# Kernel optimization log

Hardware: AMD Instinct MI355X
Metric: run time of the kernel (lower is better)

Reference implementation:

```python
import jax, jax.numpy as jnp
import numpy as np

N_OBJECTS = 32  # mask labels 1..32 (0 = background)


def setup_inputs() -> dict:
    key = jax.random.key(0)
    k1, k2, k3, k4 = jax.random.split(key, 4)
    B, F, H, W = 8, 64, 256, 256
    encoded = jax.random.normal(k1, (B, F, H, W), dtype=jnp.float32)
    masks = jax.random.randint(k2, (B, 1, H, W), 0, N_OBJECTS + 1, dtype=jnp.int32)
    W1 = jax.random.normal(k3, (2 * F, F // 2), dtype=jnp.float32) * 0.05
    b1 = jnp.zeros((F // 2,), dtype=jnp.float32)
    W2 = jax.random.normal(k4, (F // 2, 4), dtype=jnp.float32) * 0.05
    b2 = jnp.zeros((4,), dtype=jnp.float32)
    return {"encoded": encoded, "masks": masks, "W1": W1, "b1": b1, "W2": W2, "b2": b2}


def reference(encoded, masks, W1, b1, W2, b2):
    B, F, H, W = encoded.shape
    # --- masked per-object max-pool (segment max over pixels) ---
    enc = encoded.reshape(B, F, H * W).transpose(0, 2, 1)  # [B, HW, F]
    ids = masks.reshape(B, H * W)                          # [B, HW]
    seg_max = jax.vmap(
        lambda d, i: jax.ops.segment_max(d, i, num_segments=N_OBJECTS + 1)
    )(enc, ids)                                            # [B, N+1, F]
    vectors = seg_max[:, 1:, :]                            # [B, N, F] (skip label 0)

    # --- O(N^2) pairwise MLP: connections[b,c,j,i] = sigmoid(MLP([v_i; v_j])) ---
    N = vectors.shape[1]
    vi = jnp.broadcast_to(vectors[:, :, None, :], (B, N, N, F))  # v_i over axis 1
    vj = jnp.broadcast_to(vectors[:, None, :, :], (B, N, N, F))  # v_j over axis 2
    pairs = jnp.concatenate([vi, vj], axis=-1)                   # [B, N, N, 2F]
    h = jnp.einsum('bijd,dh->bijh', pairs, W1) + b1
    out = jax.nn.sigmoid(jnp.einsum('bijh,hc->bijc', h, W2) + b2)  # [B, Ni, Nj, C]
    connections = out.transpose(0, 3, 2, 1)                        # [B, C, Nj, Ni]
    return vectors, connections
```

## Files before the change

kernel.cpp:

```cpp
#include <hip/hip_runtime.h>
#include <math.h>

#define B_    8
#define F_    64
#define HW_   65536
#define NSEG  33
#define NOBJ  32
#define CHUNK 1024
#define CPB   (HW_ / CHUNK)
#define ENC_NEG_INF 0x007FFFFFu

__device__ __forceinline__ unsigned enc_f(float x) {
    unsigned u = __float_as_uint(x);
    return u ^ ((unsigned)((int)u >> 31) | 0x80000000u);
}
__device__ __forceinline__ float dec_f(unsigned e) {
    unsigned x = (e & 0x80000000u) ? (e ^ 0x80000000u) : ~e;
    return __uint_as_float(x);
}

__global__ void init_ws(unsigned* __restrict__ gws) {
    int i = blockIdx.x * blockDim.x + threadIdx.x;
    if (i < B_ * NSEG * F_) gws[i] = ENC_NEG_INF;
}

__global__ __launch_bounds__(256) void segmax_kernel(
        const float* __restrict__ enc, const int* __restrict__ masks,
        unsigned* __restrict__ gws) {
    __shared__ unsigned acc[F_ * NSEG];
    const int tid   = threadIdx.x;
    const int b     = blockIdx.x / CPB;
    const int chunk = blockIdx.x % CPB;

    for (int i = tid; i < F_ * NSEG; i += 256) acc[i] = ENC_NEG_INF;

    const int4 ids = ((const int4*)(masks + b * HW_ + chunk * CHUNK))[tid];
    __syncthreads();

    const float4* p = (const float4*)(enc + (size_t)b * F_ * HW_ + chunk * CHUNK) + tid;
    #pragma unroll 4
    for (int f = 0; f < F_; ++f) {
        float4 v = p[(size_t)f * (HW_ / 4)];
        unsigned* a = acc + f * NSEG;
        atomicMax(a + ids.x, enc_f(v.x));
        atomicMax(a + ids.y, enc_f(v.y));
        atomicMax(a + ids.z, enc_f(v.z));
        atomicMax(a + ids.w, enc_f(v.w));
    }
    __syncthreads();

    unsigned* gb = gws + b * (NSEG * F_);
    for (int i = tid; i < F_ * NSEG; i += 256) {
        unsigned val = acc[i];
        if (val != ENC_NEG_INF) {
            int f = i / NSEG, s = i % NSEG;
            atomicMax(gb + s * F_ + f, val);
        }
    }
}

__global__ __launch_bounds__(256) void mlp_kernel(
        const unsigned* __restrict__ gws,
        const float* __restrict__ W1, const float* __restrict__ b1,
        const float* __restrict__ W2, const float* __restrict__ b2,
        float* __restrict__ out_vec, float* __restrict__ out_conn) {
    const int b = blockIdx.x;
    const int tid = threadIdx.x;
    __shared__ float v[NOBJ * F_];
    __shared__ float Am[NOBJ * 33];
    __shared__ float Bm[NOBJ * 33];

    for (int i = tid; i < NOBJ * F_; i += 256) {
        int s = (i >> 6) + 1, f = i & 63;
        float val = dec_f(gws[b * NSEG * F_ + s * F_ + f]);
        v[i] = val;
        out_vec[b * NOBJ * F_ + i] = val;
    }
    __syncthreads();

    for (int e = tid; e < 2 * NOBJ * 32; e += 256) {
        int half = e >> 10;
        int idx  = e & 1023;
        int i = idx >> 5, k = idx & 31;
        const float* vv = v + i * F_;
        const float* w  = W1 + (half ? F_ * 32 : 0) + k;
        float s = 0.f;
        #pragma unroll
        for (int f = 0; f < F_; ++f) s = fmaf(vv[f], w[f * 32], s);
        if (half) Bm[i * 33 + k] = s;
        else      Am[i * 33 + k] = s + b1[k];
    }
    __syncthreads();

    for (int e = tid; e < NOBJ * NOBJ; e += 256) {
        int i = e >> 5, j = e & 31;
        float o0 = b2[0], o1 = b2[1], o2 = b2[2], o3 = b2[3];
        #pragma unroll
        for (int k = 0; k < 32; ++k) {
            float h = Am[i * 33 + k] + Bm[j * 33 + k];
            o0 = fmaf(h, W2[k * 4 + 0], o0);
            o1 = fmaf(h, W2[k * 4 + 1], o1);
            o2 = fmaf(h, W2[k * 4 + 2], o2);
            o3 = fmaf(h, W2[k * 4 + 3], o3);
        }
        float* oc = out_conn + (size_t)b * 4 * NOBJ * NOBJ + j * NOBJ + i;
        oc[0 * NOBJ * NOBJ] = 1.f / (1.f + expf(-o0));
        oc[1 * NOBJ * NOBJ] = 1.f / (1.f + expf(-o1));
        oc[2 * NOBJ * NOBJ] = 1.f / (1.f + expf(-o2));
        oc[3 * NOBJ * NOBJ] = 1.f / (1.f + expf(-o3));
    }
}

extern "C" void kernel_launch(void* const* d_in, const int* in_sizes, int n_in,
                              void* d_out, int out_size, void* d_ws, size_t ws_size,
                              hipStream_t stream) {
    const float* enc   = (const float*)d_in[0];
    const int*   masks = (const int*)  d_in[1];
    const float* W1    = (const float*)d_in[2];
    const float* b1    = (const float*)d_in[3];
    const float* W2    = (const float*)d_in[4];
    const float* b2    = (const float*)d_in[5];

    float* out_vec  = (float*)d_out;
    float* out_conn = out_vec + B_ * NOBJ * F_;
    unsigned* gws   = (unsigned*)d_ws;

    const int n = B_ * NSEG * F_;
    init_ws<<<(n + 255) / 256, 256, 0, stream>>>(gws);
    segmax_kernel<<<B_ * CPB, 256, 0, stream>>>(enc, masks, gws);
    mlp_kernel<<<B_, 256, 0, stream>>>(gws, W1, b1, W2, b2, out_vec, out_conn);
}
```

Before: 250.6 us.

## Split segmax over feature groups, batch loads, and skip redundant atomics

```diff
diff --git a/kernel.cpp b/kernel.cpp
--- a/kernel.cpp
+++ b/kernel.cpp
@@ -8,6 +8,8 @@
 #define NOBJ  32
 #define CHUNK 1024
 #define CPB   (HW_ / CHUNK)
+#define FPB   16
+#define FGRP  (F_ / FPB)
 #define ENC_NEG_INF 0x007FFFFFu
 
 __device__ __forceinline__ unsigned enc_f(float x) {
@@ -24,37 +26,49 @@
     if (i < B_ * NSEG * F_) gws[i] = ENC_NEG_INF;
 }
 
-__global__ __launch_bounds__(256) void segmax_kernel(
+__global__ __launch_bounds__(256, 6) void segmax_kernel(
         const float* __restrict__ enc, const int* __restrict__ masks,
         unsigned* __restrict__ gws) {
-    __shared__ unsigned acc[F_ * NSEG];
-    const int tid   = threadIdx.x;
-    const int b     = blockIdx.x / CPB;
-    const int chunk = blockIdx.x % CPB;
+    __shared__ unsigned acc[FPB * NSEG];
+    const int tid = threadIdx.x;
+    const int blk = blockIdx.x;
+    const int b     = blk >> 8;
+    const int r     = blk & 255;
+    const int chunk = r >> 2;
+    const int fg    = r & 3;
 
-    for (int i = tid; i < F_ * NSEG; i += 256) acc[i] = ENC_NEG_INF;
+    for (int i = tid; i < FPB * NSEG; i += 256) acc[i] = ENC_NEG_INF;
 
     const int4 ids = ((const int4*)(masks + b * HW_ + chunk * CHUNK))[tid];
     __syncthreads();
 
-    const float4* p = (const float4*)(enc + (size_t)b * F_ * HW_ + chunk * CHUNK) + tid;
-    #pragma unroll 4
-    for (int f = 0; f < F_; ++f) {
-        float4 v = p[(size_t)f * (HW_ / 4)];
-        unsigned* a = acc + f * NSEG;
-        atomicMax(a + ids.x, enc_f(v.x));
-        atomicMax(a + ids.y, enc_f(v.y));
-        atomicMax(a + ids.z, enc_f(v.z));
-        atomicMax(a + ids.w, enc_f(v.w));
+    const float4* p = (const float4*)(enc + (size_t)b * F_ * HW_
+                                      + (size_t)(fg * FPB) * HW_
+                                      + chunk * CHUNK) + tid;
+    for (int fo = 0; fo < FPB; fo += 8) {
+        float4 vbuf[8];
+        #pragma unroll
+        for (int u = 0; u < 8; ++u)
+            vbuf[u] = p[(size_t)(fo + u) * (HW_ / 4)];
+        #pragma unroll
+        for (int u = 0; u < 8; ++u) {
+            unsigned* a = acc + (fo + u) * NSEG;
+            unsigned e;
+            e = enc_f(vbuf[u].x); if (e > a[ids.x]) atomicMax(a + ids.x, e);
+            e = enc_f(vbuf[u].y); if (e > a[ids.y]) atomicMax(a + ids.y, e);
+            e = enc_f(vbuf[u].z); if (e > a[ids.z]) atomicMax(a + ids.z, e);
+            e = enc_f(vbuf[u].w); if (e > a[ids.w]) atomicMax(a + ids.w, e);
+        }
     }
     __syncthreads();
 
     unsigned* gb = gws + b * (NSEG * F_);
-    for (int i = tid; i < F_ * NSEG; i += 256) {
+    for (int i = tid; i < FPB * NSEG; i += 256) {
         unsigned val = acc[i];
         if (val != ENC_NEG_INF) {
-            int f = i / NSEG, s = i % NSEG;
-            atomicMax(gb + s * F_ + f, val);
+            int f = i / NSEG + fg * FPB, s = i % NSEG;
+            unsigned* cell = gb + s * F_ + f;
+            if (val > *cell) atomicMax(cell, val);
         }
     }
 }
@@ -67,8 +81,12 @@
     const int b = blockIdx.x;
     const int tid = threadIdx.x;
     __shared__ float v[NOBJ * F_];
+    __shared__ float w1s[2 * F_ * 32];
     __shared__ float Am[NOBJ * 33];
     __shared__ float Bm[NOBJ * 33];
+
+    for (int i = tid; i < 2 * F_ * 32 / 4; i += 256)
+        ((float4*)w1s)[i] = ((const float4*)W1)[i];
 
     for (int i = tid; i < NOBJ * F_; i += 256) {
         int s = (i >> 6) + 1, f = i & 63;
@@ -83,7 +101,7 @@
         int idx  = e & 1023;
         int i = idx >> 5, k = idx & 31;
         const float* vv = v + i * F_;
-        const float* w  = W1 + (half ? F_ * 32 : 0) + k;
+        const float* w  = w1s + half * (F_ * 32) + k;
         float s = 0.f;
         #pragma unroll
         for (int f = 0; f < F_; ++f) s = fmaf(vv[f], w[f * 32], s);
@@ -127,6 +145,6 @@
 
     const int n = B_ * NSEG * F_;
     init_ws<<<(n + 255) / 256, 256, 0, stream>>>(gws);
-    segmax_kernel<<<B_ * CPB, 256, 0, stream>>>(enc, masks, gws);
+    segmax_kernel<<<B_ * CPB * FGRP, 256, 0, stream>>>(enc, masks, gws);
     mlp_kernel<<<B_, 256, 0, stream>>>(gws, W1, b1, W2, b2, out_vec, out_conn);
 }
```

Result: slower. 356.7 us (+42.3%).

## Replace shared atomics with per-lane private segment-max and slice partials

Applied to the files above, without the earlier changes.

```diff
diff --git a/kernel.cpp b/kernel.cpp
--- a/kernel.cpp
+++ b/kernel.cpp
@@ -1,109 +1,134 @@
 #include <hip/hip_runtime.h>
 #include <math.h>
 
-#define B_    8
-#define F_    64
-#define HW_   65536
-#define NSEG  33
-#define NOBJ  32
-#define CHUNK 1024
-#define CPB   (HW_ / CHUNK)
-#define ENC_NEG_INF 0x007FFFFFu
-
-__device__ __forceinline__ unsigned enc_f(float x) {
-    unsigned u = __float_as_uint(x);
-    return u ^ ((unsigned)((int)u >> 31) | 0x80000000u);
-}
-__device__ __forceinline__ float dec_f(unsigned e) {
-    unsigned x = (e & 0x80000000u) ? (e ^ 0x80000000u) : ~e;
-    return __uint_as_float(x);
-}
-
-__global__ void init_ws(unsigned* __restrict__ gws) {
-    int i = blockIdx.x * blockDim.x + threadIdx.x;
-    if (i < B_ * NSEG * F_) gws[i] = ENC_NEG_INF;
-}
+#define B_      8
+#define F_      64
+#define HW_     65536
+#define NSEG    33
+#define NOBJ    32
+#define FPB     8
+#define SLICES  8
+#define PIXB    (HW_ / SLICES)
 
 __global__ __launch_bounds__(256) void segmax_kernel(
         const float* __restrict__ enc, const int* __restrict__ masks,
-        unsigned* __restrict__ gws) {
-    __shared__ unsigned acc[F_ * NSEG];
-    const int tid   = threadIdx.x;
-    const int b     = blockIdx.x / CPB;
-    const int chunk = blockIdx.x % CPB;
+        float* __restrict__ part) {
+    __shared__ float acc[FPB * NSEG * 32];
+    const int tid = threadIdx.x;
+    const int blk = blockIdx.x;
+    const int b     = blk >> 6;
+    const int fg    = (blk >> 3) & 7;
+    const int slice = blk & 7;
 
-    for (int i = tid; i < F_ * NSEG; i += 256) acc[i] = ENC_NEG_INF;
-
-    const int4 ids = ((const int4*)(masks + b * HW_ + chunk * CHUNK))[tid];
+    for (int i = tid; i < FPB * NSEG * 32; i += 256) acc[i] = -INFINITY;
     __syncthreads();
 
-    const float4* p = (const float4*)(enc + (size_t)b * F_ * HW_ + chunk * CHUNK) + tid;
-    #pragma unroll 4
-    for (int f = 0; f < F_; ++f) {
-        float4 v = p[(size_t)f * (HW_ / 4)];
-        unsigned* a = acc + f * NSEG;
-        atomicMax(a + ids.x, enc_f(v.x));
-        atomicMax(a + ids.y, enc_f(v.y));
-        atomicMax(a + ids.z, enc_f(v.z));
-        atomicMax(a + ids.w, enc_f(v.w));
+    const int fl = tid >> 5;
+    const int l  = tid & 31;
+    float* a = acc + fl * (NSEG * 32) + l;
+
+    const float4* ep = (const float4*)(enc + ((size_t)(b * F_ + fg * FPB + fl)) * HW_
+                                       + slice * PIXB) + l;
+    const int4*   mp = (const int4*)(masks + (size_t)b * HW_ + slice * PIXB) + l;
+
+    #pragma unroll 8
+    for (int c = 0; c < PIXB / 128; ++c) {
+        float4 v  = ep[c * 32];
+        int4   id = mp[c * 32];
+        float o;
+        o = a[id.x * 32]; a[id.x * 32] = fmaxf(o, v.x);
+        o = a[id.y * 32]; a[id.y * 32] = fmaxf(o, v.y);
+        o = a[id.z * 32]; a[id.z * 32] = fmaxf(o, v.z);
+        o = a[id.w * 32]; a[id.w * 32] = fmaxf(o, v.w);
     }
     __syncthreads();
 
-    unsigned* gb = gws + b * (NSEG * F_);
-    for (int i = tid; i < F_ * NSEG; i += 256) {
-        unsigned val = acc[i];
-        if (val != ENC_NEG_INF) {
-            int f = i / NSEG, s = i % NSEG;
-            atomicMax(gb + s * F_ + f, val);
+    float* dst = part + (((size_t)b * SLICES + slice) * NSEG) * F_;
+    for (int cell = tid; cell < FPB * NSEG; cell += 256) {
+        int f = cell & 7, s = cell >> 3;
+        const float* row = acc + f * (NSEG * 32) + s * 32;
+        float m = -INFINITY;
+        #pragma unroll
+        for (int k = 0; k < 32; k += 4) {
+            float4 q = *(const float4*)(row + k);
+            m = fmaxf(m, fmaxf(fmaxf(q.x, q.y), fmaxf(q.z, q.w)));
         }
+        dst[s * F_ + fg * FPB + f] = m;
     }
 }
 
 __global__ __launch_bounds__(256) void mlp_kernel(
-        const unsigned* __restrict__ gws,
+        const float* __restrict__ part,
         const float* __restrict__ W1, const float* __restrict__ b1,
         const float* __restrict__ W2, const float* __restrict__ b2,
         float* __restrict__ out_vec, float* __restrict__ out_conn) {
-    const int b = blockIdx.x;
+    const int b   = blockIdx.x >> 2;
+    const int it  = blockIdx.x & 3;
     const int tid = threadIdx.x;
-    __shared__ float v[NOBJ * F_];
-    __shared__ float Am[NOBJ * 33];
-    __shared__ float Bm[NOBJ * 33];
+    __shared__ float v[NOBJ * 65];
+    __shared__ float w1s[2 * F_ * 32];
+    __shared__ float w2s[32 * 4];
+    __shared__ float b1s[32];
+    __shared__ float Am[8 * 36];
+    __shared__ float Bm[NOBJ * 36];
 
-    for (int i = tid; i < NOBJ * F_; i += 256) {
-        int s = (i >> 6) + 1, f = i & 63;
-        float val = dec_f(gws[b * NSEG * F_ + s * F_ + f]);
-        v[i] = val;
-        out_vec[b * NOBJ * F_ + i] = val;
+    for (int i = tid; i < 2 * F_ * 32 / 4; i += 256)
+        ((float4*)w1s)[i] = ((const float4*)W1)[i];
+    if (tid < 32) { w2s[tid*4+0]=W2[tid*4+0]; w2s[tid*4+1]=W2[tid*4+1];
+                    w2s[tid*4+2]=W2[tid*4+2]; w2s[tid*4+3]=W2[tid*4+3];
+                    b1s[tid] = b1[tid]; }
+
+    for (int cell = tid; cell < NOBJ * F_; cell += 256) {
+        int s = (cell >> 6) + 1, f = cell & 63;
+        float m = -INFINITY;
+        #pragma unroll
+        for (int sl = 0; sl < SLICES; ++sl)
+            m = fmaxf(m, part[(((size_t)b * SLICES + sl) * NSEG + s) * F_ + f]);
+        v[(s - 1) * 65 + f] = m;
+        if (it == 0) out_vec[b * NOBJ * F_ + cell] = m;
     }
     __syncthreads();
 
-    for (int e = tid; e < 2 * NOBJ * 32; e += 256) {
-        int half = e >> 10;
-        int idx  = e & 1023;
-        int i = idx >> 5, k = idx & 31;
-        const float* vv = v + i * F_;
-        const float* w  = W1 + (half ? F_ * 32 : 0) + k;
-        float s = 0.f;
+    for (int d = tid; d < 320; d += 256) {
+        int kg, obj, half;
+        if (d < 64) { half = 0; obj = it * 8 + (d >> 3); kg = d & 7; }
+        else        { half = 1; obj = (d - 64) >> 3;     kg = d & 7; }
+        const float* vv = v + obj * 65;
+        const float* w  = w1s + half * (F_ * 32) + kg * 4;
+        float4 s4 = {0.f, 0.f, 0.f, 0.f};
         #pragma unroll
-        for (int f = 0; f < F_; ++f) s = fmaf(vv[f], w[f * 32], s);
-        if (half) Bm[i * 33 + k] = s;
-        else      Am[i * 33 + k] = s + b1[k];
+        for (int f = 0; f < F_; ++f) {
+            float4 wf = *(const float4*)(w + f * 32);
+            float x = vv[f];
+            s4.x = fmaf(x, wf.x, s4.x); s4.y = fmaf(x, wf.y, s4.y);
+            s4.z = fmaf(x, wf.z, s4.z); s4.w = fmaf(x, wf.w, s4.w);
+        }
+        if (half == 0) {
+            float4 bb = *(const float4*)(b1s + kg * 4);
+            s4.x += bb.x; s4.y += bb.y; s4.z += bb.z; s4.w += bb.w;
+            *(float4*)(Am + (d >> 3) * 36 + kg * 4) = s4;
+        } else {
+            *(float4*)(Bm + obj * 36 + kg * 4) = s4;
+        }
     }
     __syncthreads();
 
-    for (int e = tid; e < NOBJ * NOBJ; e += 256) {
-        int i = e >> 5, j = e & 31;
+    {
+        int i_loc = tid >> 5, j = tid & 31;
         float o0 = b2[0], o1 = b2[1], o2 = b2[2], o3 = b2[3];
         #pragma unroll
-        for (int k = 0; k < 32; ++k) {
-            float h = Am[i * 33 + k] + Bm[j * 33 + k];
-            o0 = fmaf(h, W2[k * 4 + 0], o0);
-            o1 = fmaf(h, W2[k * 4 + 1], o1);
-            o2 = fmaf(h, W2[k * 4 + 2], o2);
-            o3 = fmaf(h, W2[k * 4 + 3], o3);
+        for (int kg = 0; kg < 8; ++kg) {
+            float4 ha = *(const float4*)(Am + i_loc * 36 + kg * 4);
+            float4 hb = *(const float4*)(Bm + j * 36 + kg * 4);
+            float h0 = ha.x + hb.x, h1 = ha.y + hb.y;
+            float h2 = ha.z + hb.z, h3 = ha.w + hb.w;
+            const float* w2 = w2s + kg * 16;
+            o0 = fmaf(h0, w2[0],  fmaf(h1, w2[4],  fmaf(h2, w2[8],  fmaf(h3, w2[12], o0))));
+            o1 = fmaf(h0, w2[1],  fmaf(h1, w2[5],  fmaf(h2, w2[9],  fmaf(h3, w2[13], o1))));
+            o2 = fmaf(h0, w2[2],  fmaf(h1, w2[6],  fmaf(h2, w2[10], fmaf(h3, w2[14], o2))));
+            o3 = fmaf(h0, w2[3],  fmaf(h1, w2[7],  fmaf(h2, w2[11], fmaf(h3, w2[15], o3))));
         }
-        float* oc = out_conn + (size_t)b * 4 * NOBJ * NOBJ + j * NOBJ + i;
+        float* oc = out_conn + (size_t)b * 4 * NOBJ * NOBJ + j * NOBJ + (it * 8 + i_loc);
         oc[0 * NOBJ * NOBJ] = 1.f / (1.f + expf(-o0));
         oc[1 * NOBJ * NOBJ] = 1.f / (1.f + expf(-o1));
         oc[2 * NOBJ * NOBJ] = 1.f / (1.f + expf(-o2));
@@ -123,10 +148,8 @@
 
     float* out_vec  = (float*)d_out;
     float* out_conn = out_vec + B_ * NOBJ * F_;
-    unsigned* gws   = (unsigned*)d_ws;
+    float* part     = (float*)d_ws;
 
-    const int n = B_ * NSEG * F_;
-    init_ws<<<(n + 255) / 256, 256, 0, stream>>>(gws);
-    segmax_kernel<<<B_ * CPB, 256, 0, stream>>>(enc, masks, gws);
-    mlp_kernel<<<B_, 256, 0, stream>>>(gws, W1, b1, W2, b2, out_vec, out_conn);
+    segmax_kernel<<<B_ * SLICES * (F_ / FPB), 256, 0, stream>>>(enc, masks, part);
+    mlp_kernel<<<B_ * 4, 256, 0, stream>>>(part, W1, b1, W2, b2, out_vec, out_conn);
 }
```

Result: faster. 208.7 us (-16.7%).
